# Performance work log

Hardware: AMD Instinct MI355X
Metric: run time of the kernel (lower is better)

Reference implementation:

```python
import jax, jax.numpy as jnp
import numpy as np

N_NODES = 100000


def gcn_conv(x, W, b, src, dst, n_nodes):
    """PyG-style GCNConv: h = D^{-1/2} (A + I) D^{-1/2} (x @ W) + b.

    src/dst already include self-loops. Symmetric normalization with
    degrees computed on the destination index (in-degree incl. self-loop).
    """
    h = x @ W  # [N, out] - transform before propagate (cheap gather dim)
    deg = jax.ops.segment_sum(jnp.ones_like(dst, dtype=h.dtype), dst,
                              num_segments=n_nodes)  # [N]
    dinv = jnp.where(deg > 0, jax.lax.rsqrt(deg), 0.0)  # deg^{-1/2}, 0 for isolated
    norm = dinv[src] * dinv[dst]  # [E]
    msg = h[src] * norm[:, None]  # gather + normalize, [E, out]
    out = jax.ops.segment_sum(msg, dst, num_segments=n_nodes)  # scatter-sum
    return out + b


def setup_inputs() -> dict:
    key = jax.random.key(0)
    k1, k2, k3, k4 = jax.random.split(key, 4)
    in_dim, hidden, n_edges = 128, 32, 3200000
    x = jax.random.normal(k1, (N_NODES, in_dim), dtype=jnp.float32)
    edge_index = jax.random.randint(k2, (2, n_edges), 0, N_NODES, dtype=jnp.int64)
    W1 = jax.random.normal(k3, (in_dim, hidden), dtype=jnp.float32) / np.sqrt(in_dim)
    b1 = jnp.zeros((hidden,), dtype=jnp.float32)
    W2 = jax.random.normal(k4, (hidden, 1), dtype=jnp.float32) / np.sqrt(hidden)
    b2 = jnp.zeros((1,), dtype=jnp.float32)
    return {"x": x, "edge_index": edge_index, "W1": W1, "b1": b1,
            "W2": W2, "b2": b2}


def reference(x, edge_index, W1, b1, W2, b2):
    n = x.shape[0]
    loops = jnp.arange(n, dtype=edge_index.dtype)
    src = jnp.concatenate([edge_index[0], loops])  # add self-loops
    dst = jnp.concatenate([edge_index[1], loops])
    h = jax.nn.relu(gcn_conv(x, W1, b1, src, dst, n))
    out = jax.nn.sigmoid(gcn_conv(h, W2, b2, src, dst, n))
    return out.squeeze(-1)  # [N]
```

## Files before the change

kernel.cpp:

```cpp
#include <hip/hip_runtime.h>
#include <hip/hip_bf16.h>
#include <stdint.h>

#define IN_DIM 128
#define HID 32
#define CSHIFT 7
#define CNODES 128
#define CAP 4608
#define NPART 8
#define SUBCAP 672
#define TILE 4096
#define NBC_MAX 800
#define WS_ODD 2052

__device__ __forceinline__ float bf_lo(uint u) {
    uint t = u << 16; return *(float*)&t;
}
__device__ __forceinline__ float bf_hi(uint u) {
    uint t = u & 0xFFFF0000u; return *(float*)&t;
}

__global__ __launch_bounds__(256) void binB_kernel(const int* __restrict__ src,
                                                   const int* __restrict__ dst,
                                                   int* __restrict__ pcursor,
                                                   int* __restrict__ pbuf,
                                                   int e, int nbc) {
    __shared__ int hist[NBC_MAX];
    __shared__ int gbase[NBC_MAX];
    int part = blockIdx.x & (NPART - 1);
    int base = blockIdx.x * TILE;
    int cnt = min(TILE, e - base);
    if (cnt <= 0) return;
    for (int i = threadIdx.x; i < nbc; i += 256) hist[i] = 0;
    __syncthreads();
    for (int i = threadIdx.x; i < cnt; i += 256) {
        int d = dst[base + i];
        atomicAdd(&hist[d >> CSHIFT], 1);
    }
    __syncthreads();
    for (int i = threadIdx.x; i < nbc; i += 256) {
        int c = hist[i];
        gbase[i] = (c > 0) ? atomicAdd(&pcursor[part * nbc + i], c) : 0;
        hist[i] = 0;
    }
    __syncthreads();
    for (int i = threadIdx.x; i < cnt; i += 256) {
        int s = src[base + i];
        int d = dst[base + i];
        int bin = d >> CSHIFT;
        int slot = atomicAdd(&hist[bin], 1);
        int pos = gbase[bin] + slot;
        if (pos < SUBCAP)
            pbuf[(size_t)(part * nbc + bin) * SUBCAP + pos] = s | ((d & (CNODES - 1)) << 17);
    }
}

__global__ __launch_bounds__(256) void sortmm_kernel(const int* __restrict__ pcursor,
                                                     const int* __restrict__ pbuf,
                                                     int* __restrict__ csr,
                                                     int* __restrict__ row_beg,
                                                     int* __restrict__ row_end,
                                                     float* __restrict__ dinv_g,
                                                     const float* __restrict__ x,
                                                     const float* __restrict__ W1,
                                                     __hip_bfloat16* __restrict__ h1s,
                                                     int n, int nbc) {
    int b = blockIdx.x;
    __shared__ int sbe[CAP];
    __shared__ int hist[CNODES];
    __shared__ int offs[CNODES];
    __shared__ int cur[CNODES];
    __shared__ int scnt[NPART + 1];
    int tid = threadIdx.x;
    if (tid < 64) {
        int lane = tid;
        int c = (lane < NPART) ? min(pcursor[lane * nbc + b], SUBCAP) : 0;
        int pref = c;
#pragma unroll
        for (int m = 1; m < 8; m <<= 1) {
            int t = __shfl_up(pref, m);
            if (lane >= m) pref += t;
        }
        if (lane < NPART) scnt[lane + 1] = pref;
        if (lane == 0) scnt[0] = 0;
    }
    if (tid < CNODES) hist[tid] = 0;
    __syncthreads();
    for (int p = 0; p < NPART; p++) {
        int cnt = scnt[p + 1] - scnt[p];
        const int* seg = pbuf + (size_t)(p * nbc + b) * SUBCAP;
        int dstoff = scnt[p];
        for (int i = tid; i < cnt; i += 256) {
            int v = __builtin_nontemporal_load(seg + i);
            if (dstoff + i < CAP) {
                sbe[dstoff + i] = v;
                atomicAdd(&hist[v >> 17], 1);
            }
        }
    }
    __syncthreads();
    if (tid < 64) {
        int lane = tid;
        int b2 = lane * 2;
        int s0 = hist[b2], s1 = hist[b2 + 1];
        int lsum = s0 + s1;
        int pref = lsum;
#pragma unroll
        for (int m = 1; m < 64; m <<= 1) {
            int t = __shfl_up(pref, m);
            if (lane >= m) pref += t;
        }
        pref -= lsum;
        offs[b2] = pref;           cur[b2] = pref;
        offs[b2 + 1] = pref + s0;  cur[b2 + 1] = pref + s0;
    }
    __syncthreads();
    int total = min(scnt[NPART], CAP);
    int base = b * CAP;
    for (int i = tid; i < total; i += 256) {
        int p = sbe[i];
        int pos = atomicAdd(&cur[p >> 17], 1);
        csr[base + pos] = p & 0x1FFFF;
    }
    if (tid < CNODES) {
        int node = b * CNODES + tid;
        if (node < n) {
            int o = offs[tid], h = hist[tid];
            row_beg[node] = base + o;
            row_end[node] = base + o + h;
            dinv_g[node] = rsqrtf((float)h + 1.0f);
        }
    }
    __syncthreads();
    float* Ws = (float*)sbe;
    for (int i = tid; i < IN_DIM * HID; i += 256)
        Ws[i + ((i >= 2048) ? 4 : 0)] = W1[i];
    __syncthreads();
    int node2 = b * CNODES + (tid >> 1);
    int khalf = tid & 1;
    if (node2 >= n) return;
    float dv = rsqrtf((float)hist[tid >> 1] + 1.0f);
    float acc[HID];
#pragma unroll
    for (int j = 0; j < HID; j++) acc[j] = 0.f;
    const float4* xr = (const float4*)(x + (size_t)node2 * IN_DIM + khalf * 64);
    const float* Wh = Ws + (khalf ? WS_ODD : 0);
#pragma unroll 4
    for (int k4 = 0; k4 < 16; k4++) {
        float4 xv = xr[k4];
        int k = k4 * 4;
#pragma unroll
        for (int j = 0; j < HID; j++) {
            acc[j] += xv.x * Wh[(k + 0) * HID + j] + xv.y * Wh[(k + 1) * HID + j]
                    + xv.z * Wh[(k + 2) * HID + j] + xv.w * Wh[(k + 3) * HID + j];
        }
    }
#pragma unroll
    for (int j = 0; j < HID; j++) acc[j] += __shfl_xor(acc[j], 1);
    uint pkd[8];
    int abase = khalf * 16;
#pragma unroll
    for (int q = 0; q < 8; q++) {
        __hip_bfloat162 p2 = __float22bfloat162_rn(
            make_float2(acc[abase + 2 * q] * dv, acc[abase + 2 * q + 1] * dv));
        pkd[q] = *(uint*)&p2;
    }
    uint4* o = (uint4*)(h1s + (size_t)node2 * HID) + khalf * 2;
    o[0] = make_uint4(pkd[0], pkd[1], pkd[2], pkd[3]);
    o[1] = make_uint4(pkd[4], pkd[5], pkd[6], pkd[7]);
}

__global__ __launch_bounds__(256) void gather1_kernel(const int* __restrict__ row_beg,
                                                      const int* __restrict__ row_end,
                                                      const int* __restrict__ csr,
                                                      const float* __restrict__ dinv,
                                                      const __hip_bfloat16* __restrict__ h1s,
                                                      const float* __restrict__ b1,
                                                      const float* __restrict__ W2,
                                                      float* __restrict__ h2s, int n) {
    int wave = (blockIdx.x * 256 + threadIdx.x) >> 6;
    int gwaves = (gridDim.x * 256) >> 6;
    int lane = threadIdx.x & 63;
    int j2 = lane & 15;
    int quad = lane >> 4;
    const uint* h1u = (const uint*)h1s;
    float b1a = b1[2 * j2], b1b = b1[2 * j2 + 1];
    float w2a = W2[2 * j2], w2b = W2[2 * j2 + 1];
    for (int d = wave; d < n; d += gwaves) {
        int beg = row_beg[d], end = row_end[d];
        float a0 = 0.f, a1 = 0.f;
        int p = beg + quad;
        for (; p + 12 < end; p += 16) {
            int s0 = csr[p];
            int s1 = csr[p + 4];
            int s2 = csr[p + 8];
            int s3 = csr[p + 12];
            uint u0 = h1u[(size_t)s0 * 16 + j2];
            uint u1 = h1u[(size_t)s1 * 16 + j2];
            uint u2 = h1u[(size_t)s2 * 16 + j2];
            uint u3 = h1u[(size_t)s3 * 16 + j2];
            a0 += bf_lo(u0) + bf_lo(u1) + bf_lo(u2) + bf_lo(u3);
            a1 += bf_hi(u0) + bf_hi(u1) + bf_hi(u2) + bf_hi(u3);
        }
        for (; p < end; p += 4) {
            uint u = h1u[(size_t)csr[p] * 16 + j2];
            a0 += bf_lo(u);
            a1 += bf_hi(u);
        }
        a0 += __shfl_xor(a0, 16);  a0 += __shfl_xor(a0, 32);
        a1 += __shfl_xor(a1, 16);  a1 += __shfl_xor(a1, 32);
        float dd = dinv[d];
        uint su = h1u[(size_t)d * 16 + j2];
        float v0 = (a0 + bf_lo(su)) * dd + b1a;
        float v1 = (a1 + bf_hi(su)) * dd + b1b;
        v0 = fmaxf(v0, 0.f);
        v1 = fmaxf(v1, 0.f);
        float pv = v0 * w2a + v1 * w2b;
#pragma unroll
        for (int m = 1; m < 16; m <<= 1) pv += __shfl_xor(pv, m);
        if (lane == 0) h2s[d] = pv * dd;
    }
}

__global__ __launch_bounds__(256) void gather2_kernel(const int* __restrict__ row_beg,
                                                      const int* __restrict__ row_end,
                                                      const int* __restrict__ csr,
                                                      const float* __restrict__ dinv,
                                                      const float* __restrict__ h2s,
                                                      const float* __restrict__ b2,
                                                      float* __restrict__ out, int n) {
    int hw = (blockIdx.x * 256 + threadIdx.x) >> 5;
    int ghw = (gridDim.x * 256) >> 5;
    int l = threadIdx.x & 31;
    float bias = b2[0];
    for (int d = hw; d < n; d += ghw) {
        int beg = row_beg[d], end = row_end[d];
        float acc = 0.f;
        for (int p = beg + l; p < end; p += 32) {
            acc += h2s[csr[p]];
        }
#pragma unroll
        for (int m = 1; m < 32; m <<= 1) acc += __shfl_xor(acc, m, 32);
        if (l == 0) {
            float dd = dinv[d];
            float v = (acc + h2s[d]) * dd + bias;
            out[d] = 1.f / (1.f + expf(-v));
        }
    }
}

extern "C" void kernel_launch(void* const* d_in, const int* in_sizes, int n_in,
                              void* d_out, int out_size, void* d_ws, size_t ws_size,
                              hipStream_t stream) {
    const float* x  = (const float*)d_in[0];
    const int*   ei = (const int*)d_in[1];
    const float* W1 = (const float*)d_in[2];
    const float* b1 = (const float*)d_in[3];
    const float* W2 = (const float*)d_in[4];
    const float* b2 = (const float*)d_in[5];
    float* out = (float*)d_out;

    const int n = in_sizes[0] / IN_DIM;
    const int e = in_sizes[1] / 2;
    const int* src = ei;
    const int* dst = ei + e;
    const int nbc = (n + CNODES - 1) >> CSHIFT;

    int*   pbuf    = (int*)d_ws;
    int*   csr     = pbuf + (size_t)NPART * nbc * SUBCAP;
    __hip_bfloat16* h1s = (__hip_bfloat16*)(csr + (size_t)nbc * CAP);
    float* dinv    = (float*)(h1s + (size_t)n * HID);
    float* h2s     = dinv + n;
    int*   row_beg = (int*)(h2s + n);
    int*   row_end = row_beg + n;
    int*   pcursor = row_end + n;

    const int B = 256;
    int gBin = (e + TILE - 1) / TILE;
    int gP = 2048;
    int m  = NPART * nbc;

    hipMemsetAsync(pcursor, 0, (size_t)m * sizeof(int), stream);
    binB_kernel<<<gBin, B, 0, stream>>>(src, dst, pcursor, pbuf, e, nbc);
    sortmm_kernel<<<nbc, B, 0, stream>>>(pcursor, pbuf, csr, row_beg, row_end, dinv,
                                         x, W1, h1s, n, nbc);
    gather1_kernel<<<gP, B, 0, stream>>>(row_beg, row_end, csr, dinv, h1s, b1, W2, h2s, n);
    gather2_kernel<<<gP, B, 0, stream>>>(row_beg, row_end, csr, dinv, h2s, b2, out, n);
}
```

Before: 243.1 us.

## Drop CSR build; aggregate directly from binned edge buckets with LDS atomics

Removes the per-bucket counting sort that built a CSR with row_beg/row_end. Both aggregation passes now run one block per 128-node bucket, read the packed binned edges straight from pbuf, and accumulate into shared memory with atomics. The degree/matmul kernel is also changed to stage x and W1 in padded LDS tiles, with each thread computing 2 nodes by 8 outputs. This cuts the CSR write and its reread, but it adds LDS atomic contention and uses only about 782 blocks per aggregation kernel, which may limit latency hiding.

```diff
diff --git a/kernel.cpp b/kernel.cpp
--- a/kernel.cpp
+++ b/kernel.cpp
@@ -6,12 +6,10 @@
 #define HID 32
 #define CSHIFT 7
 #define CNODES 128
-#define CAP 4608
 #define NPART 8
 #define SUBCAP 672
 #define TILE 4096
 #define NBC_MAX 800
-#define WS_ODD 2052
 
 __device__ __forceinline__ float bf_lo(uint u) {
     uint t = u << 16; return *(float*)&t;
@@ -55,196 +53,188 @@
     }
 }
 
-__global__ __launch_bounds__(256) void sortmm_kernel(const int* __restrict__ pcursor,
-                                                     const int* __restrict__ pbuf,
-                                                     int* __restrict__ csr,
-                                                     int* __restrict__ row_beg,
-                                                     int* __restrict__ row_end,
-                                                     float* __restrict__ dinv_g,
-                                                     const float* __restrict__ x,
-                                                     const float* __restrict__ W1,
-                                                     __hip_bfloat16* __restrict__ h1s,
-                                                     int n, int nbc) {
+__global__ __launch_bounds__(256) void degmm_kernel(const int* __restrict__ pcursor,
+                                                    const int* __restrict__ pbuf,
+                                                    float* __restrict__ dinv_g,
+                                                    const float* __restrict__ x,
+                                                    const float* __restrict__ W1,
+                                                    __hip_bfloat16* __restrict__ h1s,
+                                                    int n, int nbc) {
     int b = blockIdx.x;
-    __shared__ int sbe[CAP];
+    __shared__ float Ws[IN_DIM * 36];
+    __shared__ float xs[CNODES * 36];
     __shared__ int hist[CNODES];
-    __shared__ int offs[CNODES];
-    __shared__ int cur[CNODES];
-    __shared__ int scnt[NPART + 1];
     int tid = threadIdx.x;
-    if (tid < 64) {
-        int lane = tid;
-        int c = (lane < NPART) ? min(pcursor[lane * nbc + b], SUBCAP) : 0;
-        int pref = c;
-#pragma unroll
-        for (int m = 1; m < 8; m <<= 1) {
-            int t = __shfl_up(pref, m);
-            if (lane >= m) pref += t;
-        }
-        if (lane < NPART) scnt[lane + 1] = pref;
-        if (lane == 0) scnt[0] = 0;
-    }
+    int w = tid >> 6, lane = tid & 63;
     if (tid < CNODES) hist[tid] = 0;
-    __syncthreads();
-    for (int p = 0; p < NPART; p++) {
-        int cnt = scnt[p + 1] - scnt[p];
+    for (int i = tid; i < IN_DIM * HID; i += 256)
+        Ws[(i >> 5) * 36 + (i & 31)] = W1[i];
+    __syncthreads();
+#pragma unroll
+    for (int pp = 0; pp < 2; pp++) {
+        int p = w + pp * 4;
+        int cnt = min(pcursor[p * nbc + b], SUBCAP);
         const int* seg = pbuf + (size_t)(p * nbc + b) * SUBCAP;
-        int dstoff = scnt[p];
-        for (int i = tid; i < cnt; i += 256) {
+        for (int i = lane; i < cnt; i += 64) {
             int v = __builtin_nontemporal_load(seg + i);
-            if (dstoff + i < CAP) {
-                sbe[dstoff + i] = v;
-                atomicAdd(&hist[v >> 17], 1);
+            atomicAdd(&hist[v >> 17], 1);
+        }
+    }
+    __syncthreads();
+    if (tid < CNODES) {
+        int node = b * CNODES + tid;
+        if (node < n) dinv_g[node] = rsqrtf((float)hist[tid] + 1.0f);
+    }
+    int ng = tid >> 2, jg = tid & 3;
+    float acc0[8], acc1[8];
+#pragma unroll
+    for (int j = 0; j < 8; j++) { acc0[j] = 0.f; acc1[j] = 0.f; }
+    for (int kc = 0; kc < 4; kc++) {
+        __syncthreads();
+        int row = tid >> 3, f4 = tid & 7;
+        for (int rr = row; rr < CNODES; rr += 32) {
+            int node = b * CNODES + rr;
+            float4 xv = make_float4(0.f, 0.f, 0.f, 0.f);
+            if (node < n)
+                xv = *(const float4*)(x + (size_t)node * IN_DIM + kc * 32 + f4 * 4);
+            *(float4*)(xs + rr * 36 + f4 * 4) = xv;
+        }
+        __syncthreads();
+        const float* Wc = Ws + kc * 32 * 36;
+#pragma unroll
+        for (int k4 = 0; k4 < 8; k4++) {
+            float4 xv0 = *(const float4*)(xs + ng * 36 + k4 * 4);
+            float4 xv1 = *(const float4*)(xs + (ng + 64) * 36 + k4 * 4);
+#pragma unroll
+            for (int kk = 0; kk < 4; kk++) {
+                const float* wr = Wc + (k4 * 4 + kk) * 36 + jg * 8;
+                float xk0 = (&xv0.x)[kk];
+                float xk1 = (&xv1.x)[kk];
+#pragma unroll
+                for (int j = 0; j < 8; j++) {
+                    float wv = wr[j];
+                    acc0[j] += xk0 * wv;
+                    acc1[j] += xk1 * wv;
+                }
             }
         }
     }
-    __syncthreads();
-    if (tid < 64) {
-        int lane = tid;
-        int b2 = lane * 2;
-        int s0 = hist[b2], s1 = hist[b2 + 1];
-        int lsum = s0 + s1;
-        int pref = lsum;
-#pragma unroll
-        for (int m = 1; m < 64; m <<= 1) {
-            int t = __shfl_up(pref, m);
-            if (lane >= m) pref += t;
-        }
-        pref -= lsum;
-        offs[b2] = pref;           cur[b2] = pref;
-        offs[b2 + 1] = pref + s0;  cur[b2 + 1] = pref + s0;
-    }
-    __syncthreads();
-    int total = min(scnt[NPART], CAP);
-    int base = b * CAP;
-    for (int i = tid; i < total; i += 256) {
-        int p = sbe[i];
-        int pos = atomicAdd(&cur[p >> 17], 1);
-        csr[base + pos] = p & 0x1FFFF;
-    }
+    int node0 = b * CNODES + ng, node1 = node0 + 64;
+    float dv0 = rsqrtf((float)hist[ng] + 1.0f);
+    float dv1 = rsqrtf((float)hist[ng + 64] + 1.0f);
+    uint pk[4];
+    if (node0 < n) {
+#pragma unroll
+        for (int q = 0; q < 4; q++) {
+            __hip_bfloat162 p2 = __float22bfloat162_rn(
+                make_float2(acc0[2 * q] * dv0, acc0[2 * q + 1] * dv0));
+            pk[q] = *(uint*)&p2;
+        }
+        ((uint4*)(h1s + (size_t)node0 * HID))[jg] = make_uint4(pk[0], pk[1], pk[2], pk[3]);
+    }
+    if (node1 < n) {
+#pragma unroll
+        for (int q = 0; q < 4; q++) {
+            __hip_bfloat162 p2 = __float22bfloat162_rn(
+                make_float2(acc1[2 * q] * dv1, acc1[2 * q + 1] * dv1));
+            pk[q] = *(uint*)&p2;
+        }
+        ((uint4*)(h1s + (size_t)node1 * HID))[jg] = make_uint4(pk[0], pk[1], pk[2], pk[3]);
+    }
+}
+
+__global__ __launch_bounds__(512) void agg1_kernel(const int* __restrict__ pcursor,
+                                                   const int* __restrict__ pbuf,
+                                                   const float* __restrict__ dinv,
+                                                   const __hip_bfloat16* __restrict__ h1s,
+                                                   const float* __restrict__ b1,
+                                                   const float* __restrict__ W2,
+                                                   float* __restrict__ h2s, int n, int nbc) {
+    int b = blockIdx.x;
+    __shared__ float acc[CNODES * 33];
+    int tid = threadIdx.x;
+    const uint* h1u = (const uint*)h1s;
+    {
+        int row = tid >> 4, u = tid & 15;
+        for (int rr = row; rr < CNODES; rr += 32) {
+            int node = b * CNODES + rr;
+            uint uv = (node < n) ? h1u[(size_t)node * 16 + u] : 0u;
+            acc[rr * 33 + 2 * u]     = bf_lo(uv);
+            acc[rr * 33 + 2 * u + 1] = bf_hi(uv);
+        }
+    }
+    __syncthreads();
+    int w = tid >> 6;
+    int lane = tid & 63;
+    int g = lane >> 4, j2 = lane & 15;
+    int cnt = min(pcursor[w * nbc + b], SUBCAP);
+    const int* seg = pbuf + (size_t)(w * nbc + b) * SUBCAP;
+    int i = g;
+    for (; i + 12 < cnt; i += 16) {
+        int v0 = seg[i], v1 = seg[i + 4], v2 = seg[i + 8], v3 = seg[i + 12];
+        uint u0 = h1u[(size_t)(v0 & 0x1FFFF) * 16 + j2];
+        uint u1 = h1u[(size_t)(v1 & 0x1FFFF) * 16 + j2];
+        uint u2 = h1u[(size_t)(v2 & 0x1FFFF) * 16 + j2];
+        uint u3 = h1u[(size_t)(v3 & 0x1FFFF) * 16 + j2];
+        atomicAdd(&acc[(v0 >> 17) * 33 + 2 * j2],     bf_lo(u0));
+        atomicAdd(&acc[(v0 >> 17) * 33 + 2 * j2 + 1], bf_hi(u0));
+        atomicAdd(&acc[(v1 >> 17) * 33 + 2 * j2],     bf_lo(u1));
+        atomicAdd(&acc[(v1 >> 17) * 33 + 2 * j2 + 1], bf_hi(u1));
+        atomicAdd(&acc[(v2 >> 17) * 33 + 2 * j2],     bf_lo(u2));
+        atomicAdd(&acc[(v2 >> 17) * 33 + 2 * j2 + 1], bf_hi(u2));
+        atomicAdd(&acc[(v3 >> 17) * 33 + 2 * j2],     bf_lo(u3));
+        atomicAdd(&acc[(v3 >> 17) * 33 + 2 * j2 + 1], bf_hi(u3));
+    }
+    for (; i < cnt; i += 4) {
+        int v = seg[i];
+        uint u = h1u[(size_t)(v & 0x1FFFF) * 16 + j2];
+        atomicAdd(&acc[(v >> 17) * 33 + 2 * j2],     bf_lo(u));
+        atomicAdd(&acc[(v >> 17) * 33 + 2 * j2 + 1], bf_hi(u));
+    }
+    __syncthreads();
+    int node_l = tid >> 2, jp = tid & 3;
+    int node = b * CNODES + node_l;
+    if (node < n) {
+        float dd = dinv[node];
+        float pv = 0.f;
+#pragma unroll
+        for (int q = 0; q < 8; q++) {
+            int j = jp * 8 + q;
+            float v = acc[node_l * 33 + j] * dd + b1[j];
+            v = fmaxf(v, 0.f);
+            pv += v * W2[j];
+        }
+        pv += __shfl_xor(pv, 1);
+        pv += __shfl_xor(pv, 2);
+        if (jp == 0) h2s[node] = pv * dd;
+    }
+}
+
+__global__ __launch_bounds__(512) void agg2_kernel(const int* __restrict__ pcursor,
+                                                   const int* __restrict__ pbuf,
+                                                   const float* __restrict__ dinv,
+                                                   const float* __restrict__ h2s,
+                                                   const float* __restrict__ b2,
+                                                   float* __restrict__ out, int n, int nbc) {
+    int b = blockIdx.x;
+    __shared__ float acc2[CNODES];
+    int tid = threadIdx.x;
+    if (tid < CNODES) acc2[tid] = 0.f;
+    __syncthreads();
+    int w = tid >> 6;
+    int lane = tid & 63;
+    int cnt = min(pcursor[w * nbc + b], SUBCAP);
+    const int* seg = pbuf + (size_t)(w * nbc + b) * SUBCAP;
+    for (int i = lane; i < cnt; i += 64) {
+        int v = seg[i];
+        atomicAdd(&acc2[v >> 17], h2s[v & 0x1FFFF]);
+    }
+    __syncthreads();
     if (tid < CNODES) {
         int node = b * CNODES + tid;
         if (node < n) {
-            int o = offs[tid], h = hist[tid];
-            row_beg[node] = base + o;
-            row_end[node] = base + o + h;
-            dinv_g[node] = rsqrtf((float)h + 1.0f);
-        }
-    }
-    __syncthreads();
-    float* Ws = (float*)sbe;
-    for (int i = tid; i < IN_DIM * HID; i += 256)
-        Ws[i + ((i >= 2048) ? 4 : 0)] = W1[i];
-    __syncthreads();
-    int node2 = b * CNODES + (tid >> 1);
-    int khalf = tid & 1;
-    if (node2 >= n) return;
-    float dv = rsqrtf((float)hist[tid >> 1] + 1.0f);
-    float acc[HID];
-#pragma unroll
-    for (int j = 0; j < HID; j++) acc[j] = 0.f;
-    const float4* xr = (const float4*)(x + (size_t)node2 * IN_DIM + khalf * 64);
-    const float* Wh = Ws + (khalf ? WS_ODD : 0);
-#pragma unroll 4
-    for (int k4 = 0; k4 < 16; k4++) {
-        float4 xv = xr[k4];
-        int k = k4 * 4;
-#pragma unroll
-        for (int j = 0; j < HID; j++) {
-            acc[j] += xv.x * Wh[(k + 0) * HID + j] + xv.y * Wh[(k + 1) * HID + j]
-                    + xv.z * Wh[(k + 2) * HID + j] + xv.w * Wh[(k + 3) * HID + j];
-        }
-    }
-#pragma unroll
-    for (int j = 0; j < HID; j++) acc[j] += __shfl_xor(acc[j], 1);
-    uint pkd[8];
-    int abase = khalf * 16;
-#pragma unroll
-    for (int q = 0; q < 8; q++) {
-        __hip_bfloat162 p2 = __float22bfloat162_rn(
-            make_float2(acc[abase + 2 * q] * dv, acc[abase + 2 * q + 1] * dv));
-        pkd[q] = *(uint*)&p2;
-    }
-    uint4* o = (uint4*)(h1s + (size_t)node2 * HID) + khalf * 2;
-    o[0] = make_uint4(pkd[0], pkd[1], pkd[2], pkd[3]);
-    o[1] = make_uint4(pkd[4], pkd[5], pkd[6], pkd[7]);
-}
-
-__global__ __launch_bounds__(256) void gather1_kernel(const int* __restrict__ row_beg,
-                                                      const int* __restrict__ row_end,
-                                                      const int* __restrict__ csr,
-                                                      const float* __restrict__ dinv,
-                                                      const __hip_bfloat16* __restrict__ h1s,
-                                                      const float* __restrict__ b1,
-                                                      const float* __restrict__ W2,
-                                                      float* __restrict__ h2s, int n) {
-    int wave = (blockIdx.x * 256 + threadIdx.x) >> 6;
-    int gwaves = (gridDim.x * 256) >> 6;
-    int lane = threadIdx.x & 63;
-    int j2 = lane & 15;
-    int quad = lane >> 4;
-    const uint* h1u = (const uint*)h1s;
-    float b1a = b1[2 * j2], b1b = b1[2 * j2 + 1];
-    float w2a = W2[2 * j2], w2b = W2[2 * j2 + 1];
-    for (int d = wave; d < n; d += gwaves) {
-        int beg = row_beg[d], end = row_end[d];
-        float a0 = 0.f, a1 = 0.f;
-        int p = beg + quad;
-        for (; p + 12 < end; p += 16) {
-            int s0 = csr[p];
-            int s1 = csr[p + 4];
-            int s2 = csr[p + 8];
-            int s3 = csr[p + 12];
-            uint u0 = h1u[(size_t)s0 * 16 + j2];
-            uint u1 = h1u[(size_t)s1 * 16 + j2];
-            uint u2 = h1u[(size_t)s2 * 16 + j2];
-            uint u3 = h1u[(size_t)s3 * 16 + j2];
-            a0 += bf_lo(u0) + bf_lo(u1) + bf_lo(u2) + bf_lo(u3);
-            a1 += bf_hi(u0) + bf_hi(u1) + bf_hi(u2) + bf_hi(u3);
-        }
-        for (; p < end; p += 4) {
-            uint u = h1u[(size_t)csr[p] * 16 + j2];
-            a0 += bf_lo(u);
-            a1 += bf_hi(u);
-        }
-        a0 += __shfl_xor(a0, 16);  a0 += __shfl_xor(a0, 32);
-        a1 += __shfl_xor(a1, 16);  a1 += __shfl_xor(a1, 32);
-        float dd = dinv[d];
-        uint su = h1u[(size_t)d * 16 + j2];
-        float v0 = (a0 + bf_lo(su)) * dd + b1a;
-        float v1 = (a1 + bf_hi(su)) * dd + b1b;
-        v0 = fmaxf(v0, 0.f);
-        v1 = fmaxf(v1, 0.f);
-        float pv = v0 * w2a + v1 * w2b;
-#pragma unroll
-        for (int m = 1; m < 16; m <<= 1) pv += __shfl_xor(pv, m);
-        if (lane == 0) h2s[d] = pv * dd;
-    }
-}
-
-__global__ __launch_bounds__(256) void gather2_kernel(const int* __restrict__ row_beg,
-                                                      const int* __restrict__ row_end,
-                                                      const int* __restrict__ csr,
-                                                      const float* __restrict__ dinv,
-                                                      const float* __restrict__ h2s,
-                                                      const float* __restrict__ b2,
-                                                      float* __restrict__ out, int n) {
-    int hw = (blockIdx.x * 256 + threadIdx.x) >> 5;
-    int ghw = (gridDim.x * 256) >> 5;
-    int l = threadIdx.x & 31;
-    float bias = b2[0];
-    for (int d = hw; d < n; d += ghw) {
-        int beg = row_beg[d], end = row_end[d];
-        float acc = 0.f;
-        for (int p = beg + l; p < end; p += 32) {
-            acc += h2s[csr[p]];
-        }
-#pragma unroll
-        for (int m = 1; m < 32; m <<= 1) acc += __shfl_xor(acc, m, 32);
-        if (l == 0) {
-            float dd = dinv[d];
-            float v = (acc + h2s[d]) * dd + bias;
-            out[d] = 1.f / (1.f + expf(-v));
+            float val = (acc2[tid] + h2s[node]) * dinv[node] + b2[0];
+            out[node] = 1.f / (1.f + expf(-val));
         }
     }
 }
@@ -266,24 +256,19 @@
     const int* dst = ei + e;
     const int nbc = (n + CNODES - 1) >> CSHIFT;
 
-    int*   pbuf    = (int*)d_ws;
-    int*   csr     = pbuf + (size_t)NPART * nbc * SUBCAP;
-    __hip_bfloat16* h1s = (__hip_bfloat16*)(csr + (size_t)nbc * CAP);
+    int* pbuf = (int*)d_ws;
+    __hip_bfloat16* h1s = (__hip_bfloat16*)(pbuf + (size_t)NPART * nbc * SUBCAP);
     float* dinv    = (float*)(h1s + (size_t)n * HID);
     float* h2s     = dinv + n;
-    int*   row_beg = (int*)(h2s + n);
-    int*   row_end = row_beg + n;
-    int*   pcursor = row_end + n;
+    int*   pcursor = (int*)(h2s + n);
 
     const int B = 256;
     int gBin = (e + TILE - 1) / TILE;
-    int gP = 2048;
     int m  = NPART * nbc;
 
     hipMemsetAsync(pcursor, 0, (size_t)m * sizeof(int), stream);
     binB_kernel<<<gBin, B, 0, stream>>>(src, dst, pcursor, pbuf, e, nbc);
-    sortmm_kernel<<<nbc, B, 0, stream>>>(pcursor, pbuf, csr, row_beg, row_end, dinv,
-                                         x, W1, h1s, n, nbc);
-    gather1_kernel<<<gP, B, 0, stream>>>(row_beg, row_end, csr, dinv, h1s, b1, W2, h2s, n);
-    gather2_kernel<<<gP, B, 0, stream>>>(row_beg, row_end, csr, dinv, h2s, b2, out, n);
-}
+    degmm_kernel<<<nbc, B, 0, stream>>>(pcursor, pbuf, dinv, x, W1, h1s, n, nbc);
+    agg1_kernel<<<nbc, 512, 0, stream>>>(pcursor, pbuf, dinv, h1s, b1, W2, h2s, n, nbc);
+    agg2_kernel<<<nbc, 512, 0, stream>>>(pcursor, pbuf, dinv, h2s, b2, out, n, nbc);
+}
```

Result: slower. 859.2 us (+253.4%).
